# Kernel optimization log

Measured on AMD Instinct MI355X. Metric: run time of the kernel, lower is better.

## Reference

```python
import math
import jax, jax.numpy as jnp
import numpy as np

B, CIN, Hh, Ww = 8, 3, 64, 64
D_MODEL = 512
N_STATE = 64
N2 = N_STATE // 2
N_LAYERS = 4
LATENT = 256
L = Hh * Ww  # 4096
EPS = 1e-5


def setup_inputs() -> dict:
    key = jax.random.key(0)
    ks = jax.random.split(key, 12)
    x = jax.random.normal(ks[0], (B, CIN, Hh, Ww), jnp.float32)
    Wproj = jax.random.normal(ks[1], (D_MODEL, CIN), jnp.float32) * (1.0 / math.sqrt(CIN))
    bproj = jnp.zeros((D_MODEL,), jnp.float32)
    pos_emb = jax.random.normal(ks[2], (1, L, D_MODEL), jnp.float32)
    # S4D kernel params (stacked over layers), per minimal S4D init
    log_dt = jax.random.uniform(ks[3], (N_LAYERS, D_MODEL), jnp.float32) * (math.log(0.1) - math.log(0.001)) + math.log(0.001)
    log_A_real = jnp.full((N_LAYERS, D_MODEL, N2), math.log(0.5), jnp.float32)
    A_imag = jnp.broadcast_to(math.pi * jnp.arange(N2, dtype=jnp.float32), (N_LAYERS, D_MODEL, N2)) + jnp.zeros((N_LAYERS, D_MODEL, N2), jnp.float32)
    C_re = jax.random.normal(ks[4], (N_LAYERS, D_MODEL, N2), jnp.float32) * (0.5 ** 0.5)
    C_im = jax.random.normal(ks[5], (N_LAYERS, D_MODEL, N2), jnp.float32) * (0.5 ** 0.5)
    Dskip = jax.random.normal(ks[6], (N_LAYERS, D_MODEL), jnp.float32)
    Wout = jax.random.normal(ks[7], (N_LAYERS, 2 * D_MODEL, D_MODEL), jnp.float32) * (1.0 / math.sqrt(D_MODEL))
    bout = jnp.zeros((N_LAYERS, 2 * D_MODEL), jnp.float32)
    ln_g = jnp.ones((N_LAYERS, D_MODEL), jnp.float32)
    ln_b = jnp.zeros((N_LAYERS, D_MODEL), jnp.float32)
    Wstats = jax.random.normal(ks[8], (2 * LATENT, D_MODEL), jnp.float32) * (1.0 / math.sqrt(D_MODEL))
    bstats = jnp.zeros((2 * LATENT,), jnp.float32)
    return dict(x=x, Wproj=Wproj, bproj=bproj, pos_emb=pos_emb, log_dt=log_dt,
                log_A_real=log_A_real, A_imag=A_imag, C_re=C_re, C_im=C_im,
                Dskip=Dskip, Wout=Wout, bout=bout, ln_g=ln_g, ln_b=ln_b,
                Wstats=Wstats, bstats=bstats)


def _s4d_layer(u, log_dt, log_A_real, A_imag, C_re, C_im, Dskip, Wout, bout):
    # u: (B, H, L); diagonal SSM via Vandermonde kernel + FFT conv (minimal S4D)
    Lseq = u.shape[-1]
    dt = jnp.exp(log_dt)                              # (H,)
    A = -jnp.exp(log_A_real) + 1j * A_imag            # (H, N2)
    dtA = A * dt[:, None]                             # (H, N2)
    Cc = (C_re + 1j * C_im) * (jnp.exp(dtA) - 1.0) / A
    t = jnp.arange(Lseq, dtype=jnp.float32)
    K = 2.0 * jnp.einsum('hn,hnl->hl', Cc, jnp.exp(dtA[:, :, None] * t)).real  # (H, L)
    k_f = jnp.fft.rfft(K, n=2 * Lseq)                 # (H, L+1)
    u_f = jnp.fft.rfft(u, n=2 * Lseq)                 # (B, H, L+1)
    y = jnp.fft.irfft(u_f * k_f, n=2 * Lseq)[..., :Lseq]
    y = y + u * Dskip[:, None]
    y = jax.nn.gelu(y, approximate=False)
    # 1x1 conv to 2H then GLU over channel dim
    y2 = jnp.einsum('oh,bhl->bol', Wout, y) + bout[:, None]
    a, b = jnp.split(y2, 2, axis=1)
    return a * jax.nn.sigmoid(b)


def _layernorm(x, g, b):
    # x: (B, L, H), normalize over H
    mu = jnp.mean(x, axis=-1, keepdims=True)
    var = jnp.mean((x - mu) ** 2, axis=-1, keepdims=True)
    return (x - mu) * jax.lax.rsqrt(var + EPS) * g + b


def reference(x, Wproj, bproj, pos_emb, log_dt, log_A_real, A_imag, C_re, C_im,
              Dskip, Wout, bout, ln_g, ln_b, Wstats, bstats):
    Bx = x.shape[0]
    # 1x1 Conv2d input projection
    h = jnp.einsum('oc,bchw->bohw', Wproj, x) + bproj[None, :, None, None]
    h = h.reshape(Bx, D_MODEL, L).transpose(0, 2, 1)  # (B, L, D)
    h = h + pos_emb
    h = h.transpose(0, 2, 1)                          # (B, D, L)
    for i in range(N_LAYERS):
        z = _s4d_layer(h, log_dt[i], log_A_real[i], A_imag[i], C_re[i], C_im[i],
                       Dskip[i], Wout[i], bout[i])
        h = h + z                                     # residual (dropout = identity at eval)
        h = _layernorm(h.transpose(0, 2, 1), ln_g[i], ln_b[i]).transpose(0, 2, 1)
    h = h.mean(-1)                                    # (B, D)
    stats = h @ Wstats.T + bstats
    mu, log_sig = jnp.split(stats, 2, axis=-1)
    return mu, log_sig
```

## Files before the change

kernel.cpp:

```cpp
#include <hip/hip_runtime.h>
#include <hip/hip_bf16.h>
#include <hip/hip_fp16.h>
#include <cmath>

#define BATCH   8
#define D_MODEL 512
#define N2      32
#define LSEQ    4096
#define NLAYERS 4
#define CIN     3
#define NBDL    (16777216u)
#define PN      (D_MODEL * N2)
#define WN      (2 * D_MODEL * D_MODEL)

typedef __attribute__((ext_vector_type(8))) short short8;
typedef __attribute__((ext_vector_type(4))) float floatx4;

__device__ float   g_h[NBDL];
__device__ __align__(16) __hip_bfloat16 g_yb[NBDL];
__device__ __align__(16) __hip_bfloat16 g_yt[NBDL];
__device__ __align__(16) __hip_bfloat16 g_wb[NLAYERS * WN];
__device__ __align__(16) __hip_bfloat16 g_G[(size_t)NLAYERS * 512 * 6 * 4096];
__device__ float4  g_p[NLAYERS * PN];
__device__ float   g_hm[BATCH * D_MODEL];
__device__ int     g_flag;

__device__ __forceinline__ float bfbits2f(unsigned short u) {
    union { unsigned int i; float f; } x; x.i = ((unsigned int)u) << 16; return x.f;
}
__device__ __forceinline__ float halfbits2f(unsigned short u) {
    __half h; *(unsigned short*)&h = u; return __half2float(h);
}
__device__ __forceinline__ float ldin(const void* p, size_t i, int m) {
    if (m == 1) return ((const float*)p)[i];
    unsigned short u = ((const unsigned short*)p)[i];
    if (m == 0) return bfbits2f(u);
    return halfbits2f(u);
}
__device__ __forceinline__ unsigned int pk2(float a, float b) {
    __hip_bfloat16 ha = __float2bfloat16(a), hb = __float2bfloat16(b);
    unsigned short ua, ub;
    __builtin_memcpy(&ua, &ha, 2); __builtin_memcpy(&ub, &hb, 2);
    return (unsigned int)ua | ((unsigned int)ub << 16);
}
__device__ __forceinline__ void split2(float a, float b, unsigned int& hp, unsigned int& lp) {
    __hip_bfloat16 ah = __float2bfloat16(a), bh = __float2bfloat16(b);
    unsigned short ua, ub;
    __builtin_memcpy(&ua, &ah, 2); __builtin_memcpy(&ub, &bh, 2);
    hp = (unsigned int)ua | ((unsigned int)ub << 16);
    lp = pk2(a - __bfloat162float(ah), b - __bfloat162float(bh));
}
__device__ __forceinline__ unsigned short bf16u(float a) {
    __hip_bfloat16 h = __float2bfloat16(a);
    unsigned short u; __builtin_memcpy(&u, &h, 2); return u;
}
__device__ __forceinline__ float2 cpow_(float br, float bi, int e) {
    float rr = 1.f, ri = 0.f;
    while (e) {
        if (e & 1) { float t = rr * br - ri * bi; ri = rr * bi + ri * br; rr = t; }
        float t = br * br - bi * bi; bi = 2.f * br * bi; br = t;
        e >>= 1;
    }
    return make_float2(rr, ri);
}

__device__ __forceinline__ float fast_gelu(float x) {
    float z = x * 0.70710678118654752f;
    float a = fabsf(z);
    float t = __builtin_amdgcn_rcpf(fmaf(0.3275911f, a, 1.0f));
    float p = t * fmaf(t, fmaf(t, fmaf(t, fmaf(t, 1.061405429f, -1.453152027f),
                                       1.421413741f), -0.284496736f), 0.254829592f);
    float e = __expf(-a * a);
    float er = fmaf(-p, e, 1.0f);
    er = copysignf(er, z);
    float hx = 0.5f * x;
    return fmaf(hx, er, hx);
}

__global__ void detect_kernel(const unsigned short* a) {
    if (threadIdx.x == 0) {
        unsigned short h1 = a[1], h3 = a[3];
        int f;
        if (h1 == 0x0000 && h3 == 0x4049) f = 1;
        else if (h1 == 0x4049)            f = 0;
        else if (h1 == 0x4248)            f = 2;
        else                              f = 1;
        g_flag = f;
    }
}

__global__ __launch_bounds__(256) void sentinel_kernel(float* out, float v) {
    out[blockIdx.x * 256 + threadIdx.x] = v;
}

__global__ __launch_bounds__(256) void proj_kernel(const void* x, const void* Wproj,
                                                   const void* bproj, const void* pos) {
    const int m = g_flag;
    unsigned idx = blockIdx.x * 256 + threadIdx.x;
    int l = idx & (LSEQ - 1);
    int o = (idx >> 12) & (D_MODEL - 1);
    int b = idx >> 21;
    float acc = ldin(bproj, o, m) + ldin(pos, (size_t)l * D_MODEL + o, m);
#pragma unroll
    for (int c = 0; c < CIN; c++)
        acc = fmaf(ldin(Wproj, o * CIN + c, m),
                   ldin(x, (size_t)(b * CIN + c) * LSEQ + l, m), acc);
    g_h[idx] = acc;
}

__global__ __launch_bounds__(256) void prep_kernel(const void* log_dt, const void* log_A_real,
                                                   const void* A_imag, const void* C_re,
                                                   const void* C_im) {
    const int m = g_flag;
    int idx = blockIdx.x * 256 + threadIdx.x;
    int layer = idx >> 14;
    int i = idx & (PN - 1);
    int hh = i >> 5;
    size_t oH = (size_t)layer * D_MODEL;
    size_t oN = (size_t)layer * PN;
    float dt  = expf(ldin(log_dt, oH + hh, m));
    float a   = expf(ldin(log_A_real, oN + i, m));
    float bi  = ldin(A_imag, oN + i, m);
    float dre = -a * dt, dim = bi * dt;
    float er  = expf(dre);
    float wr  = er * cosf(dim);
    float wi  = er * sinf(dim);
    float Er  = wr - 1.0f, Ei = wi;
    float inv = 1.0f / (a * a + bi * bi);
    float Tr = (-Er * a + Ei * bi) * inv;
    float Ti = -(Er * bi + Ei * a) * inv;
    float cr = ldin(C_re, oN + i, m), ci = ldin(C_im, oN + i, m);
    float c2r = 2.0f * (cr * Tr - ci * Ti);
    float c2i = 2.0f * (cr * Ti + ci * Tr);
    g_p[idx] = make_float4(wr, wi, c2r, c2i);
}

__global__ __launch_bounds__(256) void pack_w_kernel(const void* Wout) {
    int idx = blockIdx.x * 256 + threadIdx.x;
    g_wb[idx] = __float2bfloat16(ldin(Wout, idx, g_flag));
}

__global__ __launch_bounds__(256) void gmat_kernel() {
    __shared__ float4 psh[32];
    __shared__ unsigned short Khi[64], Klo[64];
    __shared__ __align__(16) unsigned short sC[2][64][72];
    float (*Kpart)[64] = (float(*)[64])&sC[0][0][0];
    int tid = threadIdx.x;
    int bid = blockIdx.x;
    int layer = bid >> 9, h = bid & 511;
    if (tid < 32) psh[tid] = g_p[(size_t)layer * PN + h * N2 + tid];
    __syncthreads();
    if (tid < 128) {
        int n = tid >> 2, dseg = (tid & 3) * 16;
        float4 pv = psh[n];
        float wr = pv.x, wi = pv.y;
        float2 wd = cpow_(wr, wi, dseg);
#pragma unroll
        for (int i = 0; i < 16; i++) {
            Kpart[n][dseg + i] = pv.z * wd.x - pv.w * wd.y;
            float t2 = wd.x * wr - wd.y * wi;
            wd.y = wd.x * wi + wd.y * wr; wd.x = t2;
        }
    }
    __syncthreads();
    if (tid < 64) {
        float acc = 0.f;
#pragma unroll
        for (int n = 0; n < 32; n++) acc += Kpart[n][tid];
        unsigned short khu = bf16u(acc);
        Khi[tid] = khu;
        Klo[tid] = bf16u(acc - bfbits2f(khu));
    }
    __syncthreads();
    unsigned short* Gu = (unsigned short*)(g_G + (size_t)bid * 6 * 4096);
    int t = tid >> 2, jseg = (tid & 3) * 16;
    {
        unsigned int mh[8], ml[8];
#pragma unroll
        for (int i2 = 0; i2 < 8; i2++) {
            int d0 = t - jseg - 2 * i2;
            int d1 = d0 - 1;
            unsigned int h0 = (d0 >= 0) ? (unsigned int)Khi[d0] : 0u;
            unsigned int h1 = (d1 >= 0) ? (unsigned int)Khi[d1] : 0u;
            unsigned int l0v = (d0 >= 0) ? (unsigned int)Klo[d0] : 0u;
            unsigned int l1v = (d1 >= 0) ? (unsigned int)Klo[d1] : 0u;
            mh[i2] = h0 | (h1 << 16);
            ml[i2] = l0v | (l1v << 16);
        }
        uint4 v;
        v.x = mh[0]; v.y = mh[1]; v.z = mh[2]; v.w = mh[3];
        *(uint4*)&Gu[t * 64 + jseg] = v;
        v.x = mh[4]; v.y = mh[5]; v.z = mh[6]; v.w = mh[7];
        *(uint4*)&Gu[t * 64 + jseg + 8] = v;
        v.x = ml[0]; v.y = ml[1]; v.z = ml[2]; v.w = ml[3];
        *(uint4*)&Gu[4096 + t * 64 + jseg] = v;
        v.x = ml[4]; v.y = ml[5]; v.z = ml[6]; v.w = ml[7];
        *(uint4*)&Gu[4096 + t * 64 + jseg + 8] = v;
    }
    {
        int n = t >> 1;
        float4 pv = psh[n];
        float wr = pv.x, wi = pv.y;
        float av[16];
        float2 wd = cpow_(wr, wi, 48 - jseg);
#pragma unroll
        for (int i = 15; i >= 0; i--) {
            av[i] = (t & 1) ? wd.y : wd.x;
            float t2 = wd.x * wr - wd.y * wi;
            wd.y = wd.x * wi + wd.y * wr; wd.x = t2;
        }
        unsigned int ah[8], al[8];
#pragma unroll
        for (int i2 = 0; i2 < 8; i2++)
            split2(av[2 * i2], av[2 * i2 + 1], ah[i2], al[i2]);
        uint4 v;
        v.x = ah[0]; v.y = ah[1]; v.z = ah[2]; v.w = ah[3];
        *(uint4*)&Gu[2 * 4096 + t * 64 + jseg] = v;
        v.x = ah[4]; v.y = ah[5]; v.z = ah[6]; v.w = ah[7];
        *(uint4*)&Gu[2 * 4096 + t * 64 + jseg + 8] = v;
        v.x = al[0]; v.y = al[1]; v.z = al[2]; v.w = al[3];
        *(uint4*)&Gu[3 * 4096 + t * 64 + jseg] = v;
        v.x = al[4]; v.y = al[5]; v.z = al[6]; v.w = al[7];
        *(uint4*)&Gu[3 * 4096 + t * 64 + jseg + 8] = v;
    }
    {
        int j = tid >> 2, tseg = (tid & 3) * 16;
        int n = j >> 1;
        float4 pv = psh[n];
        float wr = pv.x, wi = pv.y;
        float2 wd = cpow_(wr, wi, tseg + 1);
#pragma unroll
        for (int i = 0; i < 16; i++) {
            float zr = pv.z * wd.x - pv.w * wd.y;
            float zi = pv.z * wd.y + pv.w * wd.x;
            float cv = (j & 1) ? -zi : zr;
            unsigned short chu = bf16u(cv);
            sC[0][tseg + i][j] = chu;
            sC[1][tseg + i][j] = bf16u(cv - bfbits2f(chu));
            float t2 = wd.x * wr - wd.y * wi;
            wd.y = wd.x * wi + wd.y * wr; wd.x = t2;
        }
    }
    __syncthreads();
    *(uint4*)&Gu[4 * 4096 + t * 64 + jseg]     = *(uint4*)&sC[0][t][jseg];
    *(uint4*)&Gu[4 * 4096 + t * 64 + jseg + 8] = *(uint4*)&sC[0][t][jseg + 8];
    *(uint4*)&Gu[5 * 4096 + t * 64 + jseg]     = *(uint4*)&sC[1][t][jseg];
    *(uint4*)&Gu[5 * 4096 + t * 64 + jseg + 8] = *(uint4*)&sC[1][t][jseg + 8];
}

__global__ __launch_bounds__(256) void ssd_kernel(const void* Dskip, int layer) {
    __shared__ unsigned short sMhi[64][72];
    __shared__ unsigned short sMlo[64][72];
    __shared__ unsigned short sAC[64][72];
    __shared__ unsigned short sUhi[64][72];
    __shared__ unsigned short sUlo[64][72];
    __shared__ float sPf[64][68];
    const int m = g_flag;
    int tid = threadIdx.x;
    int bid = blockIdx.x;
    int h = bid & 511, b = bid >> 9;
    const unsigned short* Gsrc = (const unsigned short*)g_G + (size_t)(layer * 512 + h) * 6 * 4096;

    {
        int row = tid >> 2, seg = (tid & 3) * 16;
        const unsigned short* s = Gsrc + row * 64 + seg;
        *(uint4*)&sMhi[row][seg]     = *(const uint4*)(s);
        *(uint4*)&sMhi[row][seg + 8] = *(const uint4*)(s + 8);
        *(uint4*)&sMlo[row][seg]     = *(const uint4*)(s + 4096);
        *(uint4*)&sMlo[row][seg + 8] = *(const uint4*)(s + 4096 + 8);
        *(uint4*)&sAC[row][seg]      = *(const uint4*)(s + 2 * 4096);
        *(uint4*)&sAC[row][seg + 8]  = *(const uint4*)(s + 2 * 4096 + 8);
    }
    {
        const float* ub = g_h + (size_t)(b * D_MODEL + h) * LSEQ;
        int c = tid >> 2, j0 = (tid & 3) * 16;
        const float* up = ub + c * 64 + j0;
#pragma unroll
        for (int s8 = 0; s8 < 2; s8++) {
            float4 va = *(const float4*)(up + s8 * 8);
            float4 vb = *(const float4*)(up + s8 * 8 + 4);
            uint4 H, L;
            split2(va.x, va.y, H.x, L.x);
            split2(va.z, va.w, H.y, L.y);
            split2(vb.x, vb.y, H.z, L.z);
            split2(vb.z, vb.w, H.w, L.w);
            *(uint4*)&sUhi[c][j0 + s8 * 8] = H;
            *(uint4*)&sUlo[c][j0 + s8 * 8] = L;
        }
    }
    __syncthreads();

    int lane = tid & 63, wave = tid >> 6;
    int q = lane >> 4, nm = lane & 15;
    int cidx = wave * 16 + nm;
    floatx4 zed = {0.f, 0.f, 0.f, 0.f};
    floatx4 pacc[4] = {zed, zed, zed, zed};

#pragma unroll
    for (int k0 = 0; k0 < 64; k0 += 32) {
        short8 bh = *(short8*)&sUhi[cidx][k0 + q * 8];
        short8 bl = *(short8*)&sUlo[cidx][k0 + q * 8];
#pragma unroll
        for (int mi = 0; mi < 4; mi++) {
            short8 a = *(short8*)&sAC[mi * 16 + nm][k0 + q * 8];
            pacc[mi] = __builtin_amdgcn_mfma_f32_16x16x32_bf16(a, bh, pacc[mi], 0, 0, 0);
            pacc[mi] = __builtin_amdgcn_mfma_f32_16x16x32_bf16(a, bl, pacc[mi], 0, 0, 0);
        }
    }
    __syncthreads();
    if (tid >= 128) {
        int idx = tid - 128, row = idx >> 1, seg = (idx & 1) * 32;
        const unsigned short* s = Gsrc + 3 * 4096 + row * 64 + seg;
        *(uint4*)&sAC[row][seg]      = *(const uint4*)(s);
        *(uint4*)&sAC[row][seg + 8]  = *(const uint4*)(s + 8);
        *(uint4*)&sAC[row][seg + 16] = *(const uint4*)(s + 16);
        *(uint4*)&sAC[row][seg + 24] = *(const uint4*)(s + 24);
    }
    __syncthreads();
#pragma unroll
    for (int k0 = 0; k0 < 64; k0 += 32) {
        short8 bh = *(short8*)&sUhi[cidx][k0 + q * 8];
#pragma unroll
        for (int mi = 0; mi < 4; mi++) {
            short8 a = *(short8*)&sAC[mi * 16 + nm][k0 + q * 8];
            pacc[mi] = __builtin_amdgcn_mfma_f32_16x16x32_bf16(a, bh, pacc[mi], 0, 0, 0);
        }
    }
#pragma unroll
    for (int mi = 0; mi < 4; mi++)
        *(floatx4*)&sPf[cidx][mi * 16 + q * 4] = pacc[mi];
    __syncthreads();

    if (tid < 32) {
        int n = tid;
        float4 pv = g_p[(size_t)layer * PN + h * N2 + n];
        float Wr = pv.x, Wi = pv.y;
#pragma unroll
        for (int s6 = 0; s6 < 6; s6++) { float t2 = Wr * Wr - Wi * Wi; Wi = 2.f * Wr * Wi; Wr = t2; }
        float Sr = 0.f, Si = 0.f;
        for (int c = 0; c < 64; c++) {
            unsigned int* wp = (unsigned int*)&sPf[c][0];
            unsigned int pru = wp[2 * n], piu = wp[2 * n + 1];
            float pr = __uint_as_float(pru), pi = __uint_as_float(piu);
            unsigned int shw, slw;
            split2(Sr, Si, shw, slw);
            wp[n]      = shw;
            wp[32 + n] = slw;
            float t2 = fmaf(Wr, Sr, fmaf(-Wi, Si, pr));
            Si = fmaf(Wr, Si, fmaf(Wi, Sr, pi));
            Sr = t2;
        }
    }
    if (tid >= 128) {
        int idx = tid - 128, row = idx >> 1, seg = (idx & 1) * 32;
        const unsigned short* s = Gsrc + 4 * 4096 + row * 64 + seg;
        *(uint4*)&sAC[row][seg]      = *(const uint4*)(s);
        *(uint4*)&sAC[row][seg + 8]  = *(const uint4*)(s + 8);
        *(uint4*)&sAC[row][seg + 16] = *(const uint4*)(s + 16);
        *(uint4*)&sAC[row][seg + 24] = *(const uint4*)(s + 24);
    }
    __syncthreads();

    floatx4 accA[4] = {zed, zed, zed, zed};
    floatx4 accB[4] = {zed, zed, zed, zed};
#pragma unroll
    for (int k0 = 0; k0 < 64; k0 += 32) {
        short8 bh = *(short8*)&sUhi[cidx][k0 + q * 8];
        short8 bl = *(short8*)&sUlo[cidx][k0 + q * 8];
        const unsigned short* srow = (const unsigned short*)&sPf[cidx][0];
        short8 sh = *(short8*)(srow + k0 + q * 8);
        short8 sl = *(short8*)(srow + 64 + k0 + q * 8);
#pragma unroll
        for (int mi = 0; mi < 4; mi++) {
            short8 amh = *(short8*)&sMhi[mi * 16 + nm][k0 + q * 8];
            short8 aml = *(short8*)&sMlo[mi * 16 + nm][k0 + q * 8];
            short8 ac  = *(short8*)&sAC [mi * 16 + nm][k0 + q * 8];
            accA[mi] = __builtin_amdgcn_mfma_f32_16x16x32_bf16(amh, bh, accA[mi], 0, 0, 0);
            accA[mi] = __builtin_amdgcn_mfma_f32_16x16x32_bf16(amh, bl, accA[mi], 0, 0, 0);
            accA[mi] = __builtin_amdgcn_mfma_f32_16x16x32_bf16(aml, bh, accA[mi], 0, 0, 0);
            accB[mi] = __builtin_amdgcn_mfma_f32_16x16x32_bf16(ac,  sh, accB[mi], 0, 0, 0);
            accB[mi] = __builtin_amdgcn_mfma_f32_16x16x32_bf16(ac,  sl, accB[mi], 0, 0, 0);
        }
    }
    __syncthreads();
    if (tid >= 128) {
        int idx = tid - 128, row = idx >> 1, seg = (idx & 1) * 32;
        const unsigned short* s = Gsrc + 5 * 4096 + row * 64 + seg;
        *(uint4*)&sAC[row][seg]      = *(const uint4*)(s);
        *(uint4*)&sAC[row][seg + 8]  = *(const uint4*)(s + 8);
        *(uint4*)&sAC[row][seg + 16] = *(const uint4*)(s + 16);
        *(uint4*)&sAC[row][seg + 24] = *(const uint4*)(s + 24);
    }
    __syncthreads();
#pragma unroll
    for (int k0 = 0; k0 < 64; k0 += 32) {
        const unsigned short* srow = (const unsigned short*)&sPf[cidx][0];
        short8 sh = *(short8*)(srow + k0 + q * 8);
#pragma unroll
        for (int mi = 0; mi < 4; mi++) {
            short8 ac = *(short8*)&sAC[mi * 16 + nm][k0 + q * 8];
            accB[mi] = __builtin_amdgcn_mfma_f32_16x16x32_bf16(ac, sh, accB[mi], 0, 0, 0);
        }
    }

    float dsk = ldin(Dskip, (size_t)layer * D_MODEL + h, m);
    __hip_bfloat16* yb = g_yb + (size_t)(b * D_MODEL + h) * LSEQ;
#pragma unroll
    for (int mi = 0; mi < 4; mi++) {
        int t0 = mi * 16 + q * 4;
        uint2 uh = *(uint2*)&sUhi[cidx][t0];
        uint2 ul = *(uint2*)&sUlo[cidx][t0];
        float u0 = bfbits2f((unsigned short)(uh.x & 0xFFFF)) + bfbits2f((unsigned short)(ul.x & 0xFFFF));
        float u1 = bfbits2f((unsigned short)(uh.x >> 16))    + bfbits2f((unsigned short)(ul.x >> 16));
        float u2 = bfbits2f((unsigned short)(uh.y & 0xFFFF)) + bfbits2f((unsigned short)(ul.y & 0xFFFF));
        float u3 = bfbits2f((unsigned short)(uh.y >> 16))    + bfbits2f((unsigned short)(ul.y >> 16));
        float y0 = fast_gelu(accA[mi][0] + accB[mi][0] + dsk * u0);
        float y1 = fast_gelu(accA[mi][1] + accB[mi][1] + dsk * u1);
        float y2 = fast_gelu(accA[mi][2] + accB[mi][2] + dsk * u2);
        float y3 = fast_gelu(accA[mi][3] + accB[mi][3] + dsk * u3);
        uint2 o;
        o.x = pk2(y0, y1);
        o.y = pk2(y2, y3);
        *(uint2*)&yb[cidx * 64 + t0] = o;
    }
}

__global__ __launch_bounds__(256, 4) void glu_mfma_kernel(const void* bout, int layer) {
    __shared__ __align__(16) unsigned char smem[25600];
    unsigned short (* __restrict__ Wa)[40] = (unsigned short(*)[40])(smem);
    unsigned short (* __restrict__ Wb)[40] = (unsigned short(*)[40])(smem + 2560);
    unsigned int*  __restrict__ Ytd        = (unsigned int*)(smem + 5120);
    unsigned short (* __restrict__ Zs)[264] = (unsigned short(*)[264])(smem);
    const int m = g_flag;
    int tid  = threadIdx.x;
    int wave = tid >> 6, lane = tid & 63;
    int q = lane >> 4, nm = lane & 15;
    int bid = blockIdx.x;
    int xcd = bid & 7;
    int qb  = bid >> 3;
    int rt  = qb & 15;
    int ct  = (xcd << 4) | (qb >> 4);
    int col0 = ct * 256;
    int row0 = rt * 32;
    int b  = col0 >> 12;
    int l0 = col0 & (LSEQ - 1);
    const unsigned short* __restrict__ Ybb =
        (const unsigned short*)g_yb + (size_t)b * D_MODEL * LSEQ;
    const __hip_bfloat16* __restrict__ Wbase = g_wb + (size_t)layer * WN;

    floatx4 accA[2][4], accB[2][4];
    floatx4 zed = {0.f, 0.f, 0.f, 0.f};
#pragma unroll
    for (int i = 0; i < 2; i++)
#pragma unroll
        for (int j = 0; j < 4; j++) { accA[i][j] = zed; accB[i][j] = zed; }

    int sk = (tid & 3) * 8;
    int wrow = (tid & 127) >> 2;
    int p  = tid >> 4;
    int sg = tid & 15;
    int Xw = (sg & 3) << 2;
    unsigned int rowbase = (unsigned)(sg * 16) * 20 + (unsigned)(p ^ Xw);
    int wavecol = wave * 64;

    for (int k0 = 0; k0 < D_MODEL; k0 += 32) {
        if (tid < 128)
            *(uint4*)&Wa[wrow][sk] = *(const uint4*)&Wbase[(size_t)(row0 + wrow) * D_MODEL + k0 + sk];
        else
            *(uint4*)&Wb[wrow][sk] = *(const uint4*)&Wbase[(size_t)(row0 + wrow + D_MODEL) * D_MODEL + k0 + sk];
        {
            const unsigned short* yA = Ybb + (size_t)(k0 + 2 * p) * LSEQ + l0 + sg * 16;
            uint4 a0 = *(const uint4*)yA;
            uint4 a1 = *(const uint4*)(yA + 8);
            uint4 b0 = *(const uint4*)(yA + LSEQ);
            uint4 b1 = *(const uint4*)(yA + LSEQ + 8);
#define PKW(au, bu, jj)  { \
            Ytd[rowbase + (jj) * 20]       = ((au) & 0xFFFFu) | ((bu) << 16); \
            Ytd[rowbase + ((jj) + 1) * 20] = ((au) >> 16) | ((bu) & 0xFFFF0000u); }
            PKW(a0.x, b0.x, 0)  PKW(a0.y, b0.y, 2)  PKW(a0.z, b0.z, 4)  PKW(a0.w, b0.w, 6)
            PKW(a1.x, b1.x, 8)  PKW(a1.y, b1.y, 10) PKW(a1.z, b1.z, 12) PKW(a1.w, b1.w, 14)
#undef PKW
        }
        __syncthreads();
        short8 afa[2], afb[2];
#pragma unroll
        for (int mi = 0; mi < 2; mi++) {
            afa[mi] = *(short8*)&Wa[mi * 16 + nm][q * 8];
            afb[mi] = *(short8*)&Wb[mi * 16 + nm][q * 8];
        }
#pragma unroll
        for (int ni = 0; ni < 4; ni++) {
            int r = wavecol + ni * 16 + nm;
            int Xr = ((r >> 4) & 3) << 2;
            short8 bf = *(short8*)(Ytd + r * 20 + ((q * 4) ^ Xr));
#pragma unroll
            for (int mi = 0; mi < 2; mi++) {
                accA[mi][ni] = __builtin_amdgcn_mfma_f32_16x16x32_bf16(afa[mi], bf, accA[mi][ni], 0, 0, 0);
                accB[mi][ni] = __builtin_amdgcn_mfma_f32_16x16x32_bf16(afb[mi], bf, accB[mi][ni], 0, 0, 0);
            }
        }
        __syncthreads();
    }

    size_t boff = (size_t)layer * 2 * D_MODEL;
#pragma unroll
    for (int mi = 0; mi < 2; mi++) {
#pragma unroll
        for (int r = 0; r < 4; r++) {
            int lrow = mi * 16 + q * 4 + r;
            int o = row0 + lrow;
            float ba  = ldin(bout, boff + o, m);
            float bb2 = ldin(bout, boff + o + D_MODEL, m);
#pragma unroll
            for (int ni = 0; ni < 4; ni++) {
                int lcol = wavecol + ni * 16 + nm;
                float aa = accA[mi][ni][r] + ba;
                float bv = accB[mi][ni][r] + bb2;
                float z  = aa * __builtin_amdgcn_rcpf(1.0f + __expf(-bv));
                __half hz = __float2half(z);
                unsigned short hzb;
                __builtin_memcpy(&hzb, &hz, 2);
                Zs[lrow][lcol] = hzb;
            }
        }
    }
    __syncthreads();
    unsigned short* __restrict__ Zb =
        (unsigned short*)g_yt + (size_t)b * D_MODEL * LSEQ;
    int zrow = tid >> 3;
    int zcol = (tid & 7) * 32;
    size_t gbase = (size_t)(row0 + zrow) * LSEQ + l0 + zcol;
#pragma unroll
    for (int i = 0; i < 4; i++)
        *(uint4*)&Zb[gbase + i * 8] = *(uint4*)&Zs[zrow][zcol + i * 8];
}

__global__ __launch_bounds__(256) void ln_kernel(const void* g, const void* bt, int layer) {
    __shared__ float s_sum[8][32];
    __shared__ float s_sq[8][32];
    __shared__ float s_mu[32], s_rs[32];
    const int m = g_flag;
    int tid = threadIdx.x;
    int l  = tid & 31;
    int dg = tid >> 5;
    int bl = blockIdx.x;
    int b  = bl >> 7;
    int l0 = (bl & 127) * 32;
    size_t base = (size_t)b * D_MODEL * LSEQ + l0 + l;
    float* __restrict__ hp = g_h + base + (size_t)(dg * 64) * LSEQ;
    const unsigned short* __restrict__ zp =
        (const unsigned short*)g_yt + base + (size_t)(dg * 64) * LSEQ;
    size_t goff = (size_t)layer * D_MODEL + dg * 64;
    float varr[64];
    float sum = 0.f, sq = 0.f;
#pragma unroll
    for (int i = 0; i < 64; i++) {
        float v = hp[(size_t)i * LSEQ] + halfbits2f(zp[(size_t)i * LSEQ]);
        varr[i] = v;
        sum += v; sq += v * v;
    }
    s_sum[dg][l] = sum; s_sq[dg][l] = sq;
    __syncthreads();
    if (tid < 32) {
        float s = 0.f, qq = 0.f;
#pragma unroll
        for (int gq = 0; gq < 8; gq++) { s += s_sum[gq][tid]; qq += s_sq[gq][tid]; }
        float mu = s * (1.0f / D_MODEL);
        float var = qq * (1.0f / D_MODEL) - mu * mu;
        s_mu[tid] = mu;
        s_rs[tid] = rsqrtf(var + 1e-5f);
    }
    __syncthreads();
    float mu = s_mu[l], rs = s_rs[l];
#pragma unroll
    for (int i = 0; i < 64; i++) {
        hp[(size_t)i * LSEQ] = (varr[i] - mu) * rs * ldin(g, goff + i, m) + ldin(bt, goff + i, m);
    }
}

__global__ __launch_bounds__(256) void mean_kernel() {
    int bd = blockIdx.x;
    int tid = threadIdx.x;
    const float* __restrict__ row = g_h + (size_t)bd * LSEQ;
    float s = 0.f;
    for (int l = tid; l < LSEQ; l += 256) s += row[l];
#pragma unroll
    for (int off = 32; off > 0; off >>= 1) s += __shfl_down(s, off, 64);
    __shared__ float red[4];
    if ((tid & 63) == 0) red[tid >> 6] = s;
    __syncthreads();
    if (tid == 0) g_hm[bd] = (red[0] + red[1] + red[2] + red[3]) * (1.0f / LSEQ);
}

__global__ __launch_bounds__(256) void stats_kernel(const void* Wst, const void* bst,
                                                    float* __restrict__ out) {
    const int m = g_flag;
    int idx = blockIdx.x * 256 + threadIdx.x;
    int b = idx >> 9, o = idx & (D_MODEL - 1);
    const float* __restrict__ hb = g_hm + b * D_MODEL;
    float acc = ldin(bst, o, m);
    for (int d = 0; d < D_MODEL; d++)
        acc = fmaf(hb[d], ldin(Wst, (size_t)o * D_MODEL + d, m), acc);
    int pos = (o < 256) ? (b * 256 + o) : (2048 + b * 256 + (o - 256));
    out[pos] = acc;
}

extern "C" void kernel_launch(void* const* d_in, const int* in_sizes, int n_in,
                              void* d_out, int out_size, void* d_ws, size_t ws_size,
                              hipStream_t stream) {
    static const int exp_sizes[16] = {98304, 1536, 512, 2097152, 2048, 65536, 65536,
                                      65536, 65536, 2048, 2097152, 4096, 2048, 2048,
                                      262144, 512};
    bool ok = (n_in == 16);
    if (ok) for (int i = 0; i < 16; i++) if (in_sizes[i] != exp_sizes[i]) { ok = false; break; }
    if (!ok) {
        sentinel_kernel<<<(out_size + 255) / 256, 256, 0, stream>>>((float*)d_out, 1000.0f);
        return;
    }
    if (out_size != 4096) {
        sentinel_kernel<<<(out_size + 255) / 256, 256, 0, stream>>>((float*)d_out, 300.0f);
        return;
    }

    const void* x          = d_in[0];
    const void* Wproj      = d_in[1];
    const void* bproj      = d_in[2];
    const void* pos        = d_in[3];
    const void* log_dt     = d_in[4];
    const void* log_A_real = d_in[5];
    const void* A_imag     = d_in[6];
    const void* C_re       = d_in[7];
    const void* C_im       = d_in[8];
    const void* Dskip      = d_in[9];
    const void* Wout       = d_in[10];
    const void* bout       = d_in[11];
    const void* ln_g       = d_in[12];
    const void* ln_b       = d_in[13];
    const void* Wstats     = d_in[14];
    const void* bstats     = d_in[15];

    detect_kernel<<<1, 64, 0, stream>>>((const unsigned short*)A_imag);
    proj_kernel<<<NBDL / 256, 256, 0, stream>>>(x, Wproj, bproj, pos);
    prep_kernel<<<(NLAYERS * PN) / 256, 256, 0, stream>>>(
        log_dt, log_A_real, A_imag, C_re, C_im);
    pack_w_kernel<<<(NLAYERS * WN) / 256, 256, 0, stream>>>(Wout);
    gmat_kernel<<<NLAYERS * 512, 256, 0, stream>>>();

    for (int i = 0; i < NLAYERS; i++) {
        ssd_kernel<<<BATCH * D_MODEL, 256, 0, stream>>>(Dskip, i);
        glu_mfma_kernel<<<2048, 256, 0, stream>>>(bout, i);
        ln_kernel<<<(BATCH * LSEQ) / 32, 256, 0, stream>>>(ln_g, ln_b, i);
    }

    mean_kernel<<<BATCH * D_MODEL, 256, 0, stream>>>();
    stats_kernel<<<(BATCH * D_MODEL) / 256, 256, 0, stream>>>(
        Wstats, bstats, (float*)d_out);
}
```

Measured before the change: 1.050 ms.

## Loop ssd_kernel over batch per channel and tile proj_kernel through shared memory

ssd_kernel now launches one block per channel (512 blocks instead of 4096) and loops over the 8 batch elements. The per-channel G matrices (Mhi/Mlo) and the W^64 power are loaded or computed once and reused across batches. proj_kernel is rewritten so each block transposes pos_emb tiles through shared memory, giving coalesced reads of pos and coalesced writes of g_h. The cost is far fewer blocks in ssd (512 workgroups on a large GPU, so lower occupancy and latency hiding) plus extra reloads of sAC stages and extra barriers inside the loop.

```diff
diff --git a/kernel.cpp b/kernel.cpp
--- a/kernel.cpp
+++ b/kernel.cpp
@@ -95,17 +95,37 @@
 
 __global__ __launch_bounds__(256) void proj_kernel(const void* x, const void* Wproj,
                                                    const void* bproj, const void* pos) {
+    __shared__ float T[64][65];
     const int m = g_flag;
-    unsigned idx = blockIdx.x * 256 + threadIdx.x;
-    int l = idx & (LSEQ - 1);
-    int o = (idx >> 12) & (D_MODEL - 1);
-    int b = idx >> 21;
-    float acc = ldin(bproj, o, m) + ldin(pos, (size_t)l * D_MODEL + o, m);
-#pragma unroll
-    for (int c = 0; c < CIN; c++)
-        acc = fmaf(ldin(Wproj, o * CIN + c, m),
-                   ldin(x, (size_t)(b * CIN + c) * LSEQ + l, m), acc);
-    g_h[idx] = acc;
+    int tid = threadIdx.x;
+    int bid = blockIdx.x;
+    int b  = bid >> 6;
+    int l0 = (bid & 63) * 64;
+    int l  = tid & 63;
+    int g4 = tid >> 6;
+    float xv0 = ldin(x, (size_t)(b * CIN + 0) * LSEQ + l0 + l, m);
+    float xv1 = ldin(x, (size_t)(b * CIN + 1) * LSEQ + l0 + l, m);
+    float xv2 = ldin(x, (size_t)(b * CIN + 2) * LSEQ + l0 + l, m);
+    for (int o0 = 0; o0 < D_MODEL; o0 += 64) {
+        __syncthreads();
+        int ol = tid & 63;
+#pragma unroll
+        for (int p = 0; p < 16; p++) {
+            int ll = g4 * 16 + p;
+            T[ol][ll] = ldin(pos, (size_t)(l0 + ll) * D_MODEL + o0 + ol, m);
+        }
+        __syncthreads();
+#pragma unroll
+        for (int p = 0; p < 16; p++) {
+            int oc = g4 * 16 + p;
+            int o  = o0 + oc;
+            float acc = ldin(bproj, o, m) + T[oc][l];
+            acc = fmaf(ldin(Wproj, o * CIN + 0, m), xv0, acc);
+            acc = fmaf(ldin(Wproj, o * CIN + 1, m), xv1, acc);
+            acc = fmaf(ldin(Wproj, o * CIN + 2, m), xv2, acc);
+            g_h[(size_t)(b * D_MODEL + o) * LSEQ + l0 + l] = acc;
+        }
+    }
 }
 
 __global__ __launch_bounds__(256) void prep_kernel(const void* log_dt, const void* log_A_real,
@@ -257,12 +277,12 @@
     __shared__ float sPf[64][68];
     const int m = g_flag;
     int tid = threadIdx.x;
-    int bid = blockIdx.x;
-    int h = bid & 511, b = bid >> 9;
+    int h = blockIdx.x;
     const unsigned short* Gsrc = (const unsigned short*)g_G + (size_t)(layer * 512 + h) * 6 * 4096;
 
+    int row = tid >> 2, seg = (tid & 3) * 16;
+
     {
-        int row = tid >> 2, seg = (tid & 3) * 16;
         const unsigned short* s = Gsrc + row * 64 + seg;
         *(uint4*)&sMhi[row][seg]     = *(const uint4*)(s);
         *(uint4*)&sMhi[row][seg + 8] = *(const uint4*)(s + 8);
@@ -272,9 +292,7 @@
         *(uint4*)&sAC[row][seg + 8]  = *(const uint4*)(s + 2 * 4096 + 8);
     }
     {
-        const float* ub = g_h + (size_t)(b * D_MODEL + h) * LSEQ;
-        int c = tid >> 2, j0 = (tid & 3) * 16;
-        const float* up = ub + c * 64 + j0;
+        const float* up = g_h + (size_t)h * LSEQ + row * 64 + seg;
 #pragma unroll
         for (int s8 = 0; s8 < 2; s8++) {
             float4 va = *(const float4*)(up + s8 * 8);
@@ -284,144 +302,174 @@
             split2(va.z, va.w, H.y, L.y);
             split2(vb.x, vb.y, H.z, L.z);
             split2(vb.z, vb.w, H.w, L.w);
-            *(uint4*)&sUhi[c][j0 + s8 * 8] = H;
-            *(uint4*)&sUlo[c][j0 + s8 * 8] = L;
-        }
-    }
-    __syncthreads();
+            *(uint4*)&sUhi[row][seg + s8 * 8] = H;
+            *(uint4*)&sUlo[row][seg + s8 * 8] = L;
+        }
+    }
+
+    float sWr = 0.f, sWi = 0.f;
+    if (tid < 32) {
+        float4 pv = g_p[(size_t)layer * PN + h * N2 + tid];
+        float Wr = pv.x, Wi = pv.y;
+#pragma unroll
+        for (int s6 = 0; s6 < 6; s6++) { float t2 = Wr * Wr - Wi * Wi; Wi = 2.f * Wr * Wi; Wr = t2; }
+        sWr = Wr; sWi = Wi;
+    }
+    float dsk = ldin(Dskip, (size_t)layer * D_MODEL + h, m);
 
     int lane = tid & 63, wave = tid >> 6;
     int q = lane >> 4, nm = lane & 15;
     int cidx = wave * 16 + nm;
     floatx4 zed = {0.f, 0.f, 0.f, 0.f};
-    floatx4 pacc[4] = {zed, zed, zed, zed};
-
-#pragma unroll
-    for (int k0 = 0; k0 < 64; k0 += 32) {
-        short8 bh = *(short8*)&sUhi[cidx][k0 + q * 8];
-        short8 bl = *(short8*)&sUlo[cidx][k0 + q * 8];
+
+    for (int b = 0; b < 8; b++) {
+        __syncthreads();
+        floatx4 pacc[4] = {zed, zed, zed, zed};
+#pragma unroll
+        for (int k0 = 0; k0 < 64; k0 += 32) {
+            short8 bh = *(short8*)&sUhi[cidx][k0 + q * 8];
+            short8 bl = *(short8*)&sUlo[cidx][k0 + q * 8];
+#pragma unroll
+            for (int mi = 0; mi < 4; mi++) {
+                short8 a = *(short8*)&sAC[mi * 16 + nm][k0 + q * 8];
+                pacc[mi] = __builtin_amdgcn_mfma_f32_16x16x32_bf16(a, bh, pacc[mi], 0, 0, 0);
+                pacc[mi] = __builtin_amdgcn_mfma_f32_16x16x32_bf16(a, bl, pacc[mi], 0, 0, 0);
+            }
+        }
+        __syncthreads();
+        if (tid >= 128) {
+            int idx = tid - 128, row2 = idx >> 1, seg2 = (idx & 1) * 32;
+            const unsigned short* s = Gsrc + 3 * 4096 + row2 * 64 + seg2;
+            *(uint4*)&sAC[row2][seg2]      = *(const uint4*)(s);
+            *(uint4*)&sAC[row2][seg2 + 8]  = *(const uint4*)(s + 8);
+            *(uint4*)&sAC[row2][seg2 + 16] = *(const uint4*)(s + 16);
+            *(uint4*)&sAC[row2][seg2 + 24] = *(const uint4*)(s + 24);
+        }
+        __syncthreads();
+#pragma unroll
+        for (int k0 = 0; k0 < 64; k0 += 32) {
+            short8 bh = *(short8*)&sUhi[cidx][k0 + q * 8];
+#pragma unroll
+            for (int mi = 0; mi < 4; mi++) {
+                short8 a = *(short8*)&sAC[mi * 16 + nm][k0 + q * 8];
+                pacc[mi] = __builtin_amdgcn_mfma_f32_16x16x32_bf16(a, bh, pacc[mi], 0, 0, 0);
+            }
+        }
+#pragma unroll
+        for (int mi = 0; mi < 4; mi++)
+            *(floatx4*)&sPf[cidx][mi * 16 + q * 4] = pacc[mi];
+        __syncthreads();
+
+        if (tid < 32) {
+            int n = tid;
+            float Sr = 0.f, Si = 0.f;
+            for (int c = 0; c < 64; c++) {
+                unsigned int* wp = (unsigned int*)&sPf[c][0];
+                unsigned int pru = wp[2 * n], piu = wp[2 * n + 1];
+                float pr = __uint_as_float(pru), pi = __uint_as_float(piu);
+                unsigned int shw, slw;
+                split2(Sr, Si, shw, slw);
+                wp[n]      = shw;
+                wp[32 + n] = slw;
+                float t2 = fmaf(sWr, Sr, fmaf(-sWi, Si, pr));
+                Si = fmaf(sWr, Si, fmaf(sWi, Sr, pi));
+                Sr = t2;
+            }
+        }
+        if (tid >= 128) {
+            int idx = tid - 128, row2 = idx >> 1, seg2 = (idx & 1) * 32;
+            const unsigned short* s = Gsrc + 4 * 4096 + row2 * 64 + seg2;
+            *(uint4*)&sAC[row2][seg2]      = *(const uint4*)(s);
+            *(uint4*)&sAC[row2][seg2 + 8]  = *(const uint4*)(s + 8);
+            *(uint4*)&sAC[row2][seg2 + 16] = *(const uint4*)(s + 16);
+            *(uint4*)&sAC[row2][seg2 + 24] = *(const uint4*)(s + 24);
+        }
+        __syncthreads();
+
+        floatx4 accA[4] = {zed, zed, zed, zed};
+        floatx4 accB[4] = {zed, zed, zed, zed};
+#pragma unroll
+        for (int k0 = 0; k0 < 64; k0 += 32) {
+            short8 bh = *(short8*)&sUhi[cidx][k0 + q * 8];
+            short8 bl = *(short8*)&sUlo[cidx][k0 + q * 8];
+            const unsigned short* srow = (const unsigned short*)&sPf[cidx][0];
+            short8 sh = *(short8*)(srow + k0 + q * 8);
+            short8 sl = *(short8*)(srow + 64 + k0 + q * 8);
+#pragma unroll
+            for (int mi = 0; mi < 4; mi++) {
+                short8 amh = *(short8*)&sMhi[mi * 16 + nm][k0 + q * 8];
+                short8 aml = *(short8*)&sMlo[mi * 16 + nm][k0 + q * 8];
+                short8 ac  = *(short8*)&sAC [mi * 16 + nm][k0 + q * 8];
+                accA[mi] = __builtin_amdgcn_mfma_f32_16x16x32_bf16(amh, bh, accA[mi], 0, 0, 0);
+                accA[mi] = __builtin_amdgcn_mfma_f32_16x16x32_bf16(amh, bl, accA[mi], 0, 0, 0);
+                accA[mi] = __builtin_amdgcn_mfma_f32_16x16x32_bf16(aml, bh, accA[mi], 0, 0, 0);
+                accB[mi] = __builtin_amdgcn_mfma_f32_16x16x32_bf16(ac,  sh, accB[mi], 0, 0, 0);
+                accB[mi] = __builtin_amdgcn_mfma_f32_16x16x32_bf16(ac,  sl, accB[mi], 0, 0, 0);
+            }
+        }
+        __syncthreads();
+        if (tid >= 128) {
+            int idx = tid - 128, row2 = idx >> 1, seg2 = (idx & 1) * 32;
+            const unsigned short* s = Gsrc + 5 * 4096 + row2 * 64 + seg2;
+            *(uint4*)&sAC[row2][seg2]      = *(const uint4*)(s);
+            *(uint4*)&sAC[row2][seg2 + 8]  = *(const uint4*)(s + 8);
+            *(uint4*)&sAC[row2][seg2 + 16] = *(const uint4*)(s + 16);
+            *(uint4*)&sAC[row2][seg2 + 24] = *(const uint4*)(s + 24);
+        }
+        __syncthreads();
+#pragma unroll
+        for (int k0 = 0; k0 < 64; k0 += 32) {
+            const unsigned short* srow = (const unsigned short*)&sPf[cidx][0];
+            short8 sh = *(short8*)(srow + k0 + q * 8);
+#pragma unroll
+            for (int mi = 0; mi < 4; mi++) {
+                short8 ac = *(short8*)&sAC[mi * 16 + nm][k0 + q * 8];
+                accB[mi] = __builtin_amdgcn_mfma_f32_16x16x32_bf16(ac, sh, accB[mi], 0, 0, 0);
+            }
+        }
+
+        __hip_bfloat16* yb = g_yb + (size_t)(b * D_MODEL + h) * LSEQ;
 #pragma unroll
         for (int mi = 0; mi < 4; mi++) {
-            short8 a = *(short8*)&sAC[mi * 16 + nm][k0 + q * 8];
-            pacc[mi] = __builtin_amdgcn_mfma_f32_16x16x32_bf16(a, bh, pacc[mi], 0, 0, 0);
-            pacc[mi] = __builtin_amdgcn_mfma_f32_16x16x32_bf16(a, bl, pacc[mi], 0, 0, 0);
-        }
-    }
-    __syncthreads();
-    if (tid >= 128) {
-        int idx = tid - 128, row = idx >> 1, seg = (idx & 1) * 32;
-        const unsigned short* s = Gsrc + 3 * 4096 + row * 64 + seg;
-        *(uint4*)&sAC[row][seg]      = *(const uint4*)(s);
-        *(uint4*)&sAC[row][seg + 8]  = *(const uint4*)(s + 8);
-        *(uint4*)&sAC[row][seg + 16] = *(const uint4*)(s + 16);
-        *(uint4*)&sAC[row][seg + 24] = *(const uint4*)(s + 24);
-    }
-    __syncthreads();
-#pragma unroll
-    for (int k0 = 0; k0 < 64; k0 += 32) {
-        short8 bh = *(short8*)&sUhi[cidx][k0 + q * 8];
-#pragma unroll
-        for (int mi = 0; mi < 4; mi++) {
-            short8 a = *(short8*)&sAC[mi * 16 + nm][k0 + q * 8];
-            pacc[mi] = __builtin_amdgcn_mfma_f32_16x16x32_bf16(a, bh, pacc[mi], 0, 0, 0);
-        }
-    }
-#pragma unroll
-    for (int mi = 0; mi < 4; mi++)
-        *(floatx4*)&sPf[cidx][mi * 16 + q * 4] = pacc[mi];
-    __syncthreads();
-
-    if (tid < 32) {
-        int n = tid;
-        float4 pv = g_p[(size_t)layer * PN + h * N2 + n];
-        float Wr = pv.x, Wi = pv.y;
-#pragma unroll
-        for (int s6 = 0; s6 < 6; s6++) { float t2 = Wr * Wr - Wi * Wi; Wi = 2.f * Wr * Wi; Wr = t2; }
-        float Sr = 0.f, Si = 0.f;
-        for (int c = 0; c < 64; c++) {
-            unsigned int* wp = (unsigned int*)&sPf[c][0];
-            unsigned int pru = wp[2 * n], piu = wp[2 * n + 1];
-            float pr = __uint_as_float(pru), pi = __uint_as_float(piu);
-            unsigned int shw, slw;
-            split2(Sr, Si, shw, slw);
-            wp[n]      = shw;
-            wp[32 + n] = slw;
-            float t2 = fmaf(Wr, Sr, fmaf(-Wi, Si, pr));
-            Si = fmaf(Wr, Si, fmaf(Wi, Sr, pi));
-            Sr = t2;
-        }
-    }
-    if (tid >= 128) {
-        int idx = tid - 128, row = idx >> 1, seg = (idx & 1) * 32;
-        const unsigned short* s = Gsrc + 4 * 4096 + row * 64 + seg;
-        *(uint4*)&sAC[row][seg]      = *(const uint4*)(s);
-        *(uint4*)&sAC[row][seg + 8]  = *(const uint4*)(s + 8);
-        *(uint4*)&sAC[row][seg + 16] = *(const uint4*)(s + 16);
-        *(uint4*)&sAC[row][seg + 24] = *(const uint4*)(s + 24);
-    }
-    __syncthreads();
-
-    floatx4 accA[4] = {zed, zed, zed, zed};
-    floatx4 accB[4] = {zed, zed, zed, zed};
-#pragma unroll
-    for (int k0 = 0; k0 < 64; k0 += 32) {
-        short8 bh = *(short8*)&sUhi[cidx][k0 + q * 8];
-        short8 bl = *(short8*)&sUlo[cidx][k0 + q * 8];
-        const unsigned short* srow = (const unsigned short*)&sPf[cidx][0];
-        short8 sh = *(short8*)(srow + k0 + q * 8);
-        short8 sl = *(short8*)(srow + 64 + k0 + q * 8);
-#pragma unroll
-        for (int mi = 0; mi < 4; mi++) {
-            short8 amh = *(short8*)&sMhi[mi * 16 + nm][k0 + q * 8];
-            short8 aml = *(short8*)&sMlo[mi * 16 + nm][k0 + q * 8];
-            short8 ac  = *(short8*)&sAC [mi * 16 + nm][k0 + q * 8];
-            accA[mi] = __builtin_amdgcn_mfma_f32_16x16x32_bf16(amh, bh, accA[mi], 0, 0, 0);
-            accA[mi] = __builtin_amdgcn_mfma_f32_16x16x32_bf16(amh, bl, accA[mi], 0, 0, 0);
-            accA[mi] = __builtin_amdgcn_mfma_f32_16x16x32_bf16(aml, bh, accA[mi], 0, 0, 0);
-            accB[mi] = __builtin_amdgcn_mfma_f32_16x16x32_bf16(ac,  sh, accB[mi], 0, 0, 0);
-            accB[mi] = __builtin_amdgcn_mfma_f32_16x16x32_bf16(ac,  sl, accB[mi], 0, 0, 0);
-        }
-    }
-    __syncthreads();
-    if (tid >= 128) {
-        int idx = tid - 128, row = idx >> 1, seg = (idx & 1) * 32;
-        const unsigned short* s = Gsrc + 5 * 4096 + row * 64 + seg;
-        *(uint4*)&sAC[row][seg]      = *(const uint4*)(s);
-        *(uint4*)&sAC[row][seg + 8]  = *(const uint4*)(s + 8);
-        *(uint4*)&sAC[row][seg + 16] = *(const uint4*)(s + 16);
-        *(uint4*)&sAC[row][seg + 24] = *(const uint4*)(s + 24);
-    }
-    __syncthreads();
-#pragma unroll
-    for (int k0 = 0; k0 < 64; k0 += 32) {
-        const unsigned short* srow = (const unsigned short*)&sPf[cidx][0];
-        short8 sh = *(short8*)(srow + k0 + q * 8);
-#pragma unroll
-        for (int mi = 0; mi < 4; mi++) {
-            short8 ac = *(short8*)&sAC[mi * 16 + nm][k0 + q * 8];
-            accB[mi] = __builtin_amdgcn_mfma_f32_16x16x32_bf16(ac, sh, accB[mi], 0, 0, 0);
-        }
-    }
-
-    float dsk = ldin(Dskip, (size_t)layer * D_MODEL + h, m);
-    __hip_bfloat16* yb = g_yb + (size_t)(b * D_MODEL + h) * LSEQ;
-#pragma unroll
-    for (int mi = 0; mi < 4; mi++) {
-        int t0 = mi * 16 + q * 4;
-        uint2 uh = *(uint2*)&sUhi[cidx][t0];
-        uint2 ul = *(uint2*)&sUlo[cidx][t0];
-        float u0 = bfbits2f((unsigned short)(uh.x & 0xFFFF)) + bfbits2f((unsigned short)(ul.x & 0xFFFF));
-        float u1 = bfbits2f((unsigned short)(uh.x >> 16))    + bfbits2f((unsigned short)(ul.x >> 16));
-        float u2 = bfbits2f((unsigned short)(uh.y & 0xFFFF)) + bfbits2f((unsigned short)(ul.y & 0xFFFF));
-        float u3 = bfbits2f((unsigned short)(uh.y >> 16))    + bfbits2f((unsigned short)(ul.y >> 16));
-        float y0 = fast_gelu(accA[mi][0] + accB[mi][0] + dsk * u0);
-        float y1 = fast_gelu(accA[mi][1] + accB[mi][1] + dsk * u1);
-        float y2 = fast_gelu(accA[mi][2] + accB[mi][2] + dsk * u2);
-        float y3 = fast_gelu(accA[mi][3] + accB[mi][3] + dsk * u3);
-        uint2 o;
-        o.x = pk2(y0, y1);
-        o.y = pk2(y2, y3);
-        *(uint2*)&yb[cidx * 64 + t0] = o;
+            int t0 = mi * 16 + q * 4;
+            uint2 uh = *(uint2*)&sUhi[cidx][t0];
+            uint2 ul = *(uint2*)&sUlo[cidx][t0];
+            float u0 = bfbits2f((unsigned short)(uh.x & 0xFFFF)) + bfbits2f((unsigned short)(ul.x & 0xFFFF));
+            float u1 = bfbits2f((unsigned short)(uh.x >> 16))    + bfbits2f((unsigned short)(ul.x >> 16));
+            float u2 = bfbits2f((unsigned short)(uh.y & 0xFFFF)) + bfbits2f((unsigned short)(ul.y & 0xFFFF));
+            float u3 = bfbits2f((unsigned short)(uh.y >> 16))    + bfbits2f((unsigned short)(ul.y >> 16));
+            float y0 = fast_gelu(accA[mi][0] + accB[mi][0] + dsk * u0);
+            float y1 = fast_gelu(accA[mi][1] + accB[mi][1] + dsk * u1);
+            float y2 = fast_gelu(accA[mi][2] + accB[mi][2] + dsk * u2);
+            float y3 = fast_gelu(accA[mi][3] + accB[mi][3] + dsk * u3);
+            uint2 o;
+            o.x = pk2(y0, y1);
+            o.y = pk2(y2, y3);
+            *(uint2*)&yb[cidx * 64 + t0] = o;
+        }
+        __syncthreads();
+        if (b < 7) {
+            {
+                const unsigned short* s = Gsrc + 2 * 4096 + row * 64 + seg;
+                *(uint4*)&sAC[row][seg]     = *(const uint4*)(s);
+                *(uint4*)&sAC[row][seg + 8] = *(const uint4*)(s + 8);
+            }
+            {
+                const float* up = g_h + (size_t)((b + 1) * D_MODEL + h) * LSEQ + row * 64 + seg;
+#pragma unroll
+                for (int s8 = 0; s8 < 2; s8++) {
+                    float4 va = *(const float4*)(up + s8 * 8);
+                    float4 vb = *(const float4*)(up + s8 * 8 + 4);
+                    uint4 H, L;
+                    split2(va.x, va.y, H.x, L.x);
+                    split2(va.z, va.w, H.y, L.y);
+                    split2(vb.x, vb.y, H.z, L.z);
+                    split2(vb.z, vb.w, H.w, L.w);
+                    *(uint4*)&sUhi[row][seg + s8 * 8] = H;
+                    *(uint4*)&sUlo[row][seg + s8 * 8] = L;
+                }
+            }
+        }
     }
 }
 
@@ -640,14 +688,14 @@
     const void* bstats     = d_in[15];
 
     detect_kernel<<<1, 64, 0, stream>>>((const unsigned short*)A_imag);
-    proj_kernel<<<NBDL / 256, 256, 0, stream>>>(x, Wproj, bproj, pos);
+    proj_kernel<<<BATCH * 64, 256, 0, stream>>>(x, Wproj, bproj, pos);
     prep_kernel<<<(NLAYERS * PN) / 256, 256, 0, stream>>>(
         log_dt, log_A_real, A_imag, C_re, C_im);
     pack_w_kernel<<<(NLAYERS * WN) / 256, 256, 0, stream>>>(Wout);
     gmat_kernel<<<NLAYERS * 512, 256, 0, stream>>>();
 
     for (int i = 0; i < NLAYERS; i++) {
-        ssd_kernel<<<BATCH * D_MODEL, 256, 0, stream>>>(Dskip, i);
+        ssd_kernel<<<D_MODEL, 256, 0, stream>>>(Dskip, i);
         glu_mfma_kernel<<<2048, 256, 0, stream>>>(bout, i);
         ln_kernel<<<(BATCH * LSEQ) / 32, 256, 0, stream>>>(ln_g, ln_b, i);
     }
```

Result: no change. 1.055 ms (+0.4%).
